# Performance work log

Hardware: AMD Instinct MI355X
Metric: run time of the kernel (lower is better)

Reference implementation:

```python
import jax, jax.numpy as jnp
import numpy as np

RANK = 16
ALPHA = 16.0
IN_F = 4096
OUT_F = 11008
TOKENS = 64


def setup_inputs() -> dict:
    key = jax.random.key(0)
    k_x, k_w, k_s, k_a, k_b, k_bias = jax.random.split(key, 6)
    return {
        "x": jax.random.normal(k_x, (TOKENS, IN_F), dtype=jnp.float32),
        "weight_int4": jax.random.normal(k_w, (OUT_F, IN_F), dtype=jnp.float32),
        "weight_scale": jax.random.uniform(k_s, (OUT_F,), dtype=jnp.float32),
        "lora_A": jax.random.normal(k_a, (RANK, IN_F), dtype=jnp.float32) * 0.01,
        "lora_B": jax.random.normal(k_b, (OUT_F, RANK), dtype=jnp.float32),
        "bias": jax.random.normal(k_bias, (OUT_F,), dtype=jnp.float32),
    }


def reference(x, weight_int4, weight_scale, lora_A, lora_B, bias):
    # Dequantize: per-output-channel scale.  [out, in]
    weight = weight_int4 * weight_scale[:, None]
    # LoRA delta: B @ A scaled by alpha/rank.  [out, in]
    lora_weight = (lora_B @ lora_A) * (ALPHA / RANK)
    effective_weight = weight + lora_weight
    # F.linear: x @ W^T + b  ->  [tokens, out]
    return x @ effective_weight.T + bias
```

## Files before the change

### kernel.cpp

```cpp
#include <hip/hip_runtime.h>
#include <hip/hip_bf16.h>
#include <cstdint>

#define TOK   64
#define INF   4096
#define OUTF  11008
#define KCHUNKS 128
#define QCNT  8
#define NCHB  172

using bf16x8  = __attribute__((ext_vector_type(8))) __bf16;
using floatx4 = __attribute__((ext_vector_type(4))) float;

union B8u { uint32_t u[4]; uint4 q; bf16x8 v; };

__device__ __forceinline__ uint32_t hi2(float a, float b) {
    return (__float_as_uint(a) >> 16) | (__float_as_uint(b) & 0xffff0000u);
}
__device__ __forceinline__ float losub(float x) {
    return x - __uint_as_float(__float_as_uint(x) & 0xffff0000u);
}
__device__ __forceinline__ void packW(float4 a, float4 b, B8u& wh, B8u& wl) {
    wh.u[0] = hi2(a.x, a.y);  wh.u[1] = hi2(a.z, a.w);
    wh.u[2] = hi2(b.x, b.y);  wh.u[3] = hi2(b.z, b.w);
    wl.u[0] = hi2(losub(a.x), losub(a.y));
    wl.u[1] = hi2(losub(a.z), losub(a.w));
    wl.u[2] = hi2(losub(b.x), losub(b.y));
    wl.u[3] = hi2(losub(b.z), losub(b.w));
}

__global__ __launch_bounds__(256) void k_prep(const float* __restrict__ x,
        const float* __restrict__ A,
        unsigned short* __restrict__ xh, unsigned short* __restrict__ xl,
        float* __restrict__ tm) {
    int b = blockIdx.x;
    if (b < 1024) {
        int idx  = b * 256 + threadIdx.x;
        int j    = idx & 7;
        int lane = (idx >> 3) & 63;
        int kc   = (idx >> 9) & 127;
        int mt   = idx >> 16;
        int row  = mt * 16 + (lane & 15);
        int col  = kc * 32 + ((lane >> 4) << 3) + j;
        float v  = x[(size_t)row * INF + col];
        float lo = losub(v);
        xh[idx] = (unsigned short)(__float_as_uint(v) >> 16);
        xl[idx] = (unsigned short)(__float_as_uint(lo) >> 16);
    } else {
        int bb   = b - 1024;
        int t    = bb & 63;
        int wv   = threadIdx.x >> 6, lane = threadIdx.x & 63;
        int r    = (bb >> 6) * 4 + wv;
        const float4* xr = (const float4*)(x + (size_t)t * INF);
        const float4* ar = (const float4*)(A + (size_t)r * INF);
        float s = 0.f;
#pragma unroll
        for (int i = 0; i < INF / 4 / 64; ++i) {
            float4 a = xr[lane + i * 64], c = ar[lane + i * 64];
            s += a.x * c.x + a.y * c.y + a.z * c.z + a.w * c.w;
        }
#pragma unroll
        for (int off = 32; off > 0; off >>= 1) s += __shfl_down(s, off);
        if (lane == 0) tm[t * 16 + r] = s;
    }
}

template<bool ATOMIC>
__global__ __launch_bounds__(256, 1) void k_main(const float* __restrict__ W,
        const uint4* __restrict__ xh, const uint4* __restrict__ xl,
        const float* __restrict__ scale, float* __restrict__ part,
        float* __restrict__ out) {
    __shared__ uint4 wlds[2][2048];
    __shared__ uint4 xsl [2][2048];

    int tid  = threadIdx.x;
    int lane = tid & 63;
    int wv   = tid >> 6;
    int quad = lane >> 4;
    int nb   = blockIdx.x % NCHB;
    int q    = blockIdx.x / NCHB;
    int chl  = wv * 16 + (lane & 15);
    int ch   = nb * 64 + chl;

    const int kbase = q * 512;
    int rpar = lane >> 5;
    int gg   = lane & 31;

    floatx4 acc[4] = {};

    auto stage = [&](int p, int bsel) {
#pragma unroll
        for (int t = 0; t < 8; ++t) {
            int i = wv * 8 + t;
            int r = i * 2 + rpar;
            int f = (gg - r) & 31;
            const float* src = W + (size_t)(nb * 64 + r) * INF
                             + kbase + p * 128 + f * 4;
            __builtin_amdgcn_global_load_lds(
                (const __attribute__((address_space(1))) uint32_t*)src,
                (__attribute__((address_space(3))) uint32_t*)&wlds[bsel][i * 64],
                16, 0, 0);
        }
#pragma unroll
        for (int t = 0; t < 8; ++t) {
            int j  = wv * 8 + t;
            int hl = j >> 4, mt = (j >> 2) & 3, kc = j & 3;
            const uint4* src = (hl ? xl : xh)
                + ((size_t)(mt * KCHUNKS + q * 16 + p * 4 + kc) * 64 + lane);
            __builtin_amdgcn_global_load_lds(
                (const __attribute__((address_space(1))) uint32_t*)src,
                (__attribute__((address_space(3))) uint32_t*)&xsl[bsel][j * 64],
                16, 0, 0);
        }
    };

    stage(0, 0);
    stage(1, 1);

#pragma unroll
    for (int p = 0; p < 4; ++p) {
        if (p < 3) asm volatile("s_waitcnt vmcnt(16)" ::: "memory");
        else       asm volatile("s_waitcnt vmcnt(0)"  ::: "memory");
        __builtin_amdgcn_s_barrier();
        __builtin_amdgcn_sched_barrier(0);

        const int buf = p & 1;
#pragma unroll
        for (int kc = 0; kc < 4; ++kc) {
            int f0 = (kc * 4 + quad) * 2;
            uint4 wf0 = wlds[buf][chl * 32 + ((f0 + chl) & 31)];
            uint4 wf1 = wlds[buf][chl * 32 + ((f0 + 1 + chl) & 31)];
            B8u wh, wl;
            packW(*(float4*)&wf0, *(float4*)&wf1, wh, wl);
#pragma unroll
            for (int mt = 0; mt < 4; ++mt) {
                B8u ah, al;
                ah.q = xsl[buf][(mt * 4 + kc) * 64 + lane];
                al.q = xsl[buf][(16 + mt * 4 + kc) * 64 + lane];
                acc[mt] = __builtin_amdgcn_mfma_f32_16x16x32_bf16(ah.v, wh.v, acc[mt], 0, 0, 0);
                acc[mt] = __builtin_amdgcn_mfma_f32_16x16x32_bf16(ah.v, wl.v, acc[mt], 0, 0, 0);
                acc[mt] = __builtin_amdgcn_mfma_f32_16x16x32_bf16(al.v, wh.v, acc[mt], 0, 0, 0);
            }
        }

        if (p < 2) {
            asm volatile("s_waitcnt lgkmcnt(0)" ::: "memory");
            __builtin_amdgcn_s_barrier();
            stage(p + 2, buf);
        }
    }

#pragma unroll
    for (int mt = 0; mt < 4; ++mt) {
        int token = mt * 16 + quad * 4;
#pragma unroll
        for (int r = 0; r < 4; ++r) {
            if constexpr (ATOMIC) {
                atomicAdd(&out[(size_t)(token + r) * OUTF + ch], scale[ch] * acc[mt][r]);
            } else {
                part[((size_t)q * TOK + token + r) * OUTF + ch] = acc[mt][r];
            }
        }
    }
}

__global__ __launch_bounds__(256) void k_post(const float* __restrict__ part,
        const float* __restrict__ scale, const float* __restrict__ bias,
        const float* __restrict__ lB, const float* __restrict__ tm,
        float* __restrict__ out) {
    int o = blockIdx.x * 256 + threadIdx.x;
    int t = blockIdx.y;
    if (o >= OUTF) return;
    float s = 0.f;
#pragma unroll
    for (int qq = 0; qq < QCNT; ++qq)
        s += part[((size_t)qq * TOK + t) * OUTF + o];
    const float4* Br = (const float4*)(lB + (size_t)o * 16);
    const float4* tr = (const float4*)(tm + (size_t)t * 16);
    float l = 0.f;
#pragma unroll
    for (int i = 0; i < 4; ++i) {
        float4 b = Br[i], tt = tr[i];
        l += b.x * tt.x + b.y * tt.y + b.z * tt.z + b.w * tt.w;
    }
    out[(size_t)t * OUTF + o] = s * scale[o] + l + bias[o];
}

__global__ __launch_bounds__(256) void k_pre(const float* __restrict__ bias,
        const float* __restrict__ lB, const float* __restrict__ tm,
        float* __restrict__ out) {
    int o = blockIdx.x * 256 + threadIdx.x;
    int t = blockIdx.y;
    if (o >= OUTF) return;
    const float4* Br = (const float4*)(lB + (size_t)o * 16);
    const float4* tr = (const float4*)(tm + (size_t)t * 16);
    float l = 0.f;
#pragma unroll
    for (int i = 0; i < 4; ++i) {
        float4 b = Br[i], tt = tr[i];
        l += b.x * tt.x + b.y * tt.y + b.z * tt.z + b.w * tt.w;
    }
    out[(size_t)t * OUTF + o] = l + bias[o];
}

extern "C" void kernel_launch(void* const* d_in, const int* in_sizes, int n_in,
                              void* d_out, int out_size, void* d_ws, size_t ws_size,
                              hipStream_t stream) {
    const float* x     = (const float*)d_in[0];
    const float* W     = (const float*)d_in[1];
    const float* scale = (const float*)d_in[2];
    const float* lA    = (const float*)d_in[3];
    const float* lB    = (const float*)d_in[4];
    const float* bias  = (const float*)d_in[5];
    float* out = (float*)d_out;

    char* ws = (char*)d_ws;
    unsigned short* xh = (unsigned short*)(ws);
    unsigned short* xl = (unsigned short*)(ws + 524288);
    float* tm   = (float*)(ws + 1048576);
    float* part = (float*)(ws + 1052672);
    const size_t need = 1052672 + (size_t)QCNT * TOK * OUTF * 4;

    k_prep<<<1280, 256, 0, stream>>>(x, lA, xh, xl, tm);

    if (ws_size >= need) {
        k_main<false><<<NCHB * QCNT, 256, 0, stream>>>(W, (const uint4*)xh,
                (const uint4*)xl, scale, part, out);
        k_post<<<dim3(43, TOK), 256, 0, stream>>>(part, scale, bias, lB, tm, out);
    } else {
        k_pre<<<dim3(43, TOK), 256, 0, stream>>>(bias, lB, tm, out);
        k_main<true><<<NCHB * QCNT, 256, 0, stream>>>(W, (const uint4*)xh,
                (const uint4*)xl, scale, nullptr, out);
    }
}
```

Measured before the change: 283.9 us.

## Drop split-K, run full K per block and fuse epilogue into main kernel

After: 286.0 us. No clear change (+0.8%).

```diff
diff --git a/kernel.cpp b/kernel.cpp
--- a/kernel.cpp
+++ b/kernel.cpp
@@ -6,7 +6,6 @@
 #define INF   4096
 #define OUTF  11008
 #define KCHUNKS 128
-#define QCNT  8
 #define NCHB  172
 
 using bf16x8  = __attribute__((ext_vector_type(8))) __bf16;
@@ -65,26 +64,27 @@
     }
 }
 
-template<bool ATOMIC>
 __global__ __launch_bounds__(256, 1) void k_main(const float* __restrict__ W,
         const uint4* __restrict__ xh, const uint4* __restrict__ xl,
-        const float* __restrict__ scale, float* __restrict__ part,
+        const float* __restrict__ scale, const float* __restrict__ lB,
+        const float* __restrict__ bias, const float* __restrict__ tm,
         float* __restrict__ out) {
     __shared__ uint4 wlds[2][2048];
     __shared__ uint4 xsl [2][2048];
+    __shared__ float tml[1024];
 
     int tid  = threadIdx.x;
     int lane = tid & 63;
     int wv   = tid >> 6;
     int quad = lane >> 4;
-    int nb   = blockIdx.x % NCHB;
-    int q    = blockIdx.x / NCHB;
+    int nb   = blockIdx.x;
     int chl  = wv * 16 + (lane & 15);
     int ch   = nb * 64 + chl;
 
-    const int kbase = q * 512;
     int rpar = lane >> 5;
     int gg   = lane & 31;
+
+    ((float4*)tml)[tid] = ((const float4*)tm)[tid];
 
     floatx4 acc[4] = {};
 
@@ -95,7 +95,7 @@
             int r = i * 2 + rpar;
             int f = (gg - r) & 31;
             const float* src = W + (size_t)(nb * 64 + r) * INF
-                             + kbase + p * 128 + f * 4;
+                             + p * 128 + f * 4;
             __builtin_amdgcn_global_load_lds(
                 (const __attribute__((address_space(1))) uint32_t*)src,
                 (__attribute__((address_space(3))) uint32_t*)&wlds[bsel][i * 64],
@@ -106,7 +106,7 @@
             int j  = wv * 8 + t;
             int hl = j >> 4, mt = (j >> 2) & 3, kc = j & 3;
             const uint4* src = (hl ? xl : xh)
-                + ((size_t)(mt * KCHUNKS + q * 16 + p * 4 + kc) * 64 + lane);
+                + ((size_t)(mt * KCHUNKS + p * 4 + kc) * 64 + lane);
             __builtin_amdgcn_global_load_lds(
                 (const __attribute__((address_space(1))) uint32_t*)src,
                 (__attribute__((address_space(3))) uint32_t*)&xsl[bsel][j * 64],
@@ -114,17 +114,7 @@
         }
     };
 
-    stage(0, 0);
-    stage(1, 1);
-
-#pragma unroll
-    for (int p = 0; p < 4; ++p) {
-        if (p < 3) asm volatile("s_waitcnt vmcnt(16)" ::: "memory");
-        else       asm volatile("s_waitcnt vmcnt(0)"  ::: "memory");
-        __builtin_amdgcn_s_barrier();
-        __builtin_amdgcn_sched_barrier(0);
-
-        const int buf = p & 1;
+    auto compute = [&](int buf) {
 #pragma unroll
         for (int kc = 0; kc < 4; ++kc) {
             int f0 = (kc * 4 + quad) * 2;
@@ -142,65 +132,49 @@
                 acc[mt] = __builtin_amdgcn_mfma_f32_16x16x32_bf16(al.v, wh.v, acc[mt], 0, 0, 0);
             }
         }
+    };
 
-        if (p < 2) {
-            asm volatile("s_waitcnt lgkmcnt(0)" ::: "memory");
-            __builtin_amdgcn_s_barrier();
-            stage(p + 2, buf);
+    stage(0, 0);
+    stage(1, 1);
+
+#pragma unroll 2
+    for (int p = 0; p < 30; ++p) {
+        asm volatile("s_waitcnt vmcnt(16)" ::: "memory");
+        __builtin_amdgcn_s_barrier();
+        __builtin_amdgcn_sched_barrier(0);
+        const int buf = p & 1;
+        compute(buf);
+        asm volatile("s_waitcnt lgkmcnt(0)" ::: "memory");
+        __builtin_amdgcn_s_barrier();
+        stage(p + 2, buf);
+    }
+    asm volatile("s_waitcnt vmcnt(16)" ::: "memory");
+    __builtin_amdgcn_s_barrier();
+    __builtin_amdgcn_sched_barrier(0);
+    compute(0);
+    asm volatile("s_waitcnt vmcnt(0)" ::: "memory");
+    __builtin_amdgcn_s_barrier();
+    __builtin_amdgcn_sched_barrier(0);
+    compute(1);
+
+    float sc = scale[ch];
+    float bs = bias[ch];
+    const float4* Br = (const float4*)(lB + (size_t)ch * 16);
+    float4 b0 = Br[0], b1 = Br[1], b2 = Br[2], b3 = Br[3];
+#pragma unroll
+    for (int mt = 0; mt < 4; ++mt) {
+#pragma unroll
+        for (int r = 0; r < 4; ++r) {
+            int token = mt * 16 + quad * 4 + r;
+            const float4* tt = (const float4*)&tml[token * 16];
+            float4 t0 = tt[0], t1 = tt[1], t2 = tt[2], t3 = tt[3];
+            float l = b0.x * t0.x + b0.y * t0.y + b0.z * t0.z + b0.w * t0.w
+                    + b1.x * t1.x + b1.y * t1.y + b1.z * t1.z + b1.w * t1.w
+                    + b2.x * t2.x + b2.y * t2.y + b2.z * t2.z + b2.w * t2.w
+                    + b3.x * t3.x + b3.y * t3.y + b3.z * t3.z + b3.w * t3.w;
+            out[(size_t)token * OUTF + ch] = sc * acc[mt][r] + l + bs;
         }
     }
-
-#pragma unroll
-    for (int mt = 0; mt < 4; ++mt) {
-        int token = mt * 16 + quad * 4;
-#pragma unroll
-        for (int r = 0; r < 4; ++r) {
-            if constexpr (ATOMIC) {
-                atomicAdd(&out[(size_t)(token + r) * OUTF + ch], scale[ch] * acc[mt][r]);
-            } else {
-                part[((size_t)q * TOK + token + r) * OUTF + ch] = acc[mt][r];
-            }
-        }
-    }
-}
-
-__global__ __launch_bounds__(256) void k_post(const float* __restrict__ part,
-        const float* __restrict__ scale, const float* __restrict__ bias,
-        const float* __restrict__ lB, const float* __restrict__ tm,
-        float* __restrict__ out) {
-    int o = blockIdx.x * 256 + threadIdx.x;
-    int t = blockIdx.y;
-    if (o >= OUTF) return;
-    float s = 0.f;
-#pragma unroll
-    for (int qq = 0; qq < QCNT; ++qq)
-        s += part[((size_t)qq * TOK + t) * OUTF + o];
-    const float4* Br = (const float4*)(lB + (size_t)o * 16);
-    const float4* tr = (const float4*)(tm + (size_t)t * 16);
-    float l = 0.f;
-#pragma unroll
-    for (int i = 0; i < 4; ++i) {
-        float4 b = Br[i], tt = tr[i];
-        l += b.x * tt.x + b.y * tt.y + b.z * tt.z + b.w * tt.w;
-    }
-    out[(size_t)t * OUTF + o] = s * scale[o] + l + bias[o];
-}
-
-__global__ __launch_bounds__(256) void k_pre(const float* __restrict__ bias,
-        const float* __restrict__ lB, const float* __restrict__ tm,
-        float* __restrict__ out) {
-    int o = blockIdx.x * 256 + threadIdx.x;
-    int t = blockIdx.y;
-    if (o >= OUTF) return;
-    const float4* Br = (const float4*)(lB + (size_t)o * 16);
-    const float4* tr = (const float4*)(tm + (size_t)t * 16);
-    float l = 0.f;
-#pragma unroll
-    for (int i = 0; i < 4; ++i) {
-        float4 b = Br[i], tt = tr[i];
-        l += b.x * tt.x + b.y * tt.y + b.z * tt.z + b.w * tt.w;
-    }
-    out[(size_t)t * OUTF + o] = l + bias[o];
 }
 
 extern "C" void kernel_launch(void* const* d_in, const int* in_sizes, int n_in,
@@ -218,18 +192,8 @@
     unsigned short* xh = (unsigned short*)(ws);
     unsigned short* xl = (unsigned short*)(ws + 524288);
     float* tm   = (float*)(ws + 1048576);
-    float* part = (float*)(ws + 1052672);
-    const size_t need = 1052672 + (size_t)QCNT * TOK * OUTF * 4;
 
     k_prep<<<1280, 256, 0, stream>>>(x, lA, xh, xl, tm);
-
-    if (ws_size >= need) {
-        k_main<false><<<NCHB * QCNT, 256, 0, stream>>>(W, (const uint4*)xh,
-                (const uint4*)xl, scale, part, out);
-        k_post<<<dim3(43, TOK), 256, 0, stream>>>(part, scale, bias, lB, tm, out);
-    } else {
-        k_pre<<<dim3(43, TOK), 256, 0, stream>>>(bias, lB, tm, out);
-        k_main<true><<<NCHB * QCNT, 256, 0, stream>>>(W, (const uint4*)xh,
-                (const uint4*)xl, scale, nullptr, out);
-    }
+    k_main<<<NCHB, 256, 0, stream>>>(W, (const uint4*)xh, (const uint4*)xl,
+                                     scale, lB, bias, tm, out);
 }
```
